# Optimization experiments

Measured on AMD Instinct MI355X. Metric: run time of the kernel, lower is better.

Reference implementation:

```python
import jax, jax.numpy as jnp
import numpy as np
from jax.scipy.special import logsumexp

D_MODEL = 512
NHEAD = 8
BATCH = 2
SEQ = 1024


def _safe_log_relu(v):
    # log(max(v, 0)) with well-defined (zero) gradient where v <= 0
    pos = v > 0
    return jnp.where(pos, jnp.log(jnp.where(pos, v, 1.0)), -jnp.inf)


def _split_heads(t, h):
    b, l, hd = t.shape
    return t.reshape(b, l, h, hd // h).transpose(0, 2, 1, 3)  # (B,H,L,d)


def setup_inputs() -> dict:
    key = jax.random.key(0)
    ks = jax.random.split(key, 9)
    s = 1.0 / np.sqrt(D_MODEL)
    x = jax.random.normal(ks[0], (BATCH, SEQ, D_MODEL), jnp.float32)
    mk = lambda k: jax.random.normal(k, (D_MODEL, D_MODEL), jnp.float32) * s
    mb = lambda k: jax.random.normal(k, (D_MODEL,), jnp.float32) * 0.02
    return {
        "x": x,
        "W_Q": mk(ks[1]), "b_Q": mb(ks[2]),
        "W_K": mk(ks[3]), "b_K": mb(ks[4]),
        "W_V": mk(ks[5]), "b_V": mb(ks[6]),
        "W_O": mk(ks[7]), "b_O": mb(ks[8]),
    }


def reference(x, W_Q, b_Q, W_K, b_K, W_V, b_V, W_O, b_O):
    # self-attention: queries = keys = values = x
    Q = _split_heads(x @ W_Q.T + b_Q, NHEAD)  # (B,H,L,D)
    K = _split_heads(x @ W_K.T + b_K, NHEAD)  # (B,H,L,D)
    V = _split_heads(x @ W_V.T + b_V, NHEAD)  # (B,H,L,Dv)

    # normalizer: log sum_j sum_d exp(Q_id) * exp(K_jd)
    log_B = logsumexp(Q + logsumexp(K, axis=-2, keepdims=True), axis=-1)  # (B,H,L)

    log_V_plus = _safe_log_relu(V)[..., None, :]    # (B,H,L,1,Dv)
    log_V_minus = _safe_log_relu(-V)[..., None, :]  # (B,H,L,1,Dv)

    # reduce over key positions: (B,H,L,D,Dv) -> (B,H,D,Dv)
    lse_KV_plus = logsumexp(K[..., :, :, None] + log_V_plus, axis=-3)
    lse_KV_minus = logsumexp(K[..., :, :, None] + log_V_minus, axis=-3)

    # reduce over feature dim D: (B,H,L,D,Dv) -> (B,H,L,Dv)
    log_A_plus = logsumexp(Q[..., None] + lse_KV_plus[..., None, :, :], axis=-2)
    log_A_minus = logsumexp(Q[..., None] + lse_KV_minus[..., None, :, :], axis=-2)

    heads = jnp.exp(log_A_plus - log_B[..., None]) - jnp.exp(log_A_minus - log_B[..., None])

    b, h, l, dv = heads.shape
    joined = heads.transpose(0, 2, 1, 3).reshape(b, l, h * dv)
    return joined @ W_O.T + b_O
```

## Files before the change

### kernel.cpp

```cpp
#include <hip/hip_runtime.h>
#include <math.h>

#define DM   512
#define NH   8
#define HD   64
#define B_   2
#define L_   1024
#define M_   (B_ * L_)

typedef __attribute__((ext_vector_type(8))) short  bfrag;
typedef __attribute__((ext_vector_type(4))) float  fv4;
typedef __attribute__((ext_vector_type(4))) unsigned short usv4;
typedef __attribute__((ext_vector_type(8))) unsigned short usv8;

__device__ __forceinline__ unsigned short f32_bf16_rne(float f) {
    unsigned u = __float_as_uint(f);
    unsigned r = u + 0x7FFF + ((u >> 16) & 1);
    return (unsigned short)(r >> 16);
}
__device__ __forceinline__ float bf16_f32(unsigned short h) {
    return __uint_as_float(((unsigned)h) << 16);
}

__device__ __forceinline__ void stage16(const unsigned short* g, unsigned short* l) {
    __builtin_amdgcn_global_load_lds(
        (const __attribute__((address_space(1))) void*)g,
        (__attribute__((address_space(3))) void*)l,
        16, 0, 0);
}

__global__ __launch_bounds__(256) void prep_kernel(
    const float* __restrict__ x,
    const float* __restrict__ Wq, const float* __restrict__ Wk,
    const float* __restrict__ Wv,
    unsigned short* __restrict__ xh, unsigned short* __restrict__ xl,
    unsigned short* __restrict__ wh, unsigned short* __restrict__ wl,
    float* __restrict__ zred) {
    int bid = blockIdx.x;
    if (bid >= 1792) {
        float4 zv = {0.f, 0.f, 0.f, 0.f};
        *(float4*)(zred + (size_t)threadIdx.x * 4) = zv;
        return;
    }
    const float* src; unsigned short *dh, *dl; size_t off;
    if (bid < 1024) {
        src = x; dh = xh; dl = xl; off = (size_t)bid * 1024;
    } else {
        int wsel = (bid - 1024) >> 8;
        int wb   = (bid - 1024) & 255;
        src = (wsel == 0) ? Wq : (wsel == 1) ? Wk : Wv;
        dh = wh + (size_t)wsel * 262144;
        dl = wl + (size_t)wsel * 262144;
        off = (size_t)wb * 1024;
    }
    size_t i = off + (size_t)threadIdx.x * 4;
    float4 v = *(const float4*)(src + i);
    usv4 h, l;
    h.x = f32_bf16_rne(v.x); l.x = f32_bf16_rne(v.x - bf16_f32(h.x));
    h.y = f32_bf16_rne(v.y); l.y = f32_bf16_rne(v.y - bf16_f32(h.y));
    h.z = f32_bf16_rne(v.z); l.z = f32_bf16_rne(v.z - bf16_f32(h.z));
    h.w = f32_bf16_rne(v.w); l.w = f32_bf16_rne(v.w - bf16_f32(h.w));
    *(usv4*)(dh + i) = h;
    *(usv4*)(dl + i) = l;
}

#define TM 64
#define TN 64
#define TK 32
#define LDA 32
#define NSTEP (DM / TK)

__device__ __forceinline__ void mfma_gemm_bf16(
    const unsigned short* __restrict__ Ahg, const unsigned short* __restrict__ Alg,
    const unsigned short* __restrict__ Bhg, const unsigned short* __restrict__ Blg,
    const float* __restrict__ bias, float* __restrict__ C, int do_exp,
    int m0, int n0) {
    __shared__ __align__(16) unsigned short Ah[2][TM * LDA];
    __shared__ __align__(16) unsigned short Al[2][TM * LDA];
    __shared__ __align__(16) unsigned short Bh[2][TN * LDA];
    __shared__ __align__(16) unsigned short Bl[2][TN * LDA];

    const int tid  = threadIdx.x;
    const int wave = tid >> 6, lane = tid & 63;
    const int quad = lane >> 4, r16 = lane & 15;

    const int srow = lane >> 2;
    const int scol = (lane & 3) << 3;
    const size_t gaBase = (size_t)(m0 + wave * 16 + srow) * DM + scol;
    const size_t gbBase = (size_t)(n0 + wave * 16 + srow) * DM + scol;
    const int ldst = wave * 512;

    fv4 acc[4] = {};

    stage16(Ahg + gaBase, &Ah[0][ldst]);
    stage16(Alg + gaBase, &Al[0][ldst]);
    stage16(Bhg + gbBase, &Bh[0][ldst]);
    stage16(Blg + gbBase, &Bl[0][ldst]);
    __syncthreads();

    int cur = 0;
    for (int t = 0; t < NSTEP; ++t) {
        if (t + 1 < NSTEP) {
            const size_t koff = (size_t)(t + 1) * TK;
            stage16(Ahg + gaBase + koff, &Ah[cur ^ 1][ldst]);
            stage16(Alg + gaBase + koff, &Al[cur ^ 1][ldst]);
            stage16(Bhg + gbBase + koff, &Bh[cur ^ 1][ldst]);
            stage16(Blg + gbBase + koff, &Bl[cur ^ 1][ldst]);
        }
        const int aoff = (wave * 16 + r16) * LDA + quad * 8;
        bfrag ah = *(const bfrag*)(&Ah[cur][aoff]);
        bfrag al = *(const bfrag*)(&Al[cur][aoff]);
        bfrag bh[4], bl[4];
#pragma unroll
        for (int j = 0; j < 4; ++j) {
            const int boff = (j * 16 + r16) * LDA + quad * 8;
            bh[j] = *(const bfrag*)(&Bh[cur][boff]);
            bl[j] = *(const bfrag*)(&Bl[cur][boff]);
        }
#pragma unroll
        for (int j = 0; j < 4; ++j) {
            acc[j] = __builtin_amdgcn_mfma_f32_16x16x32_bf16(ah, bh[j], acc[j], 0, 0, 0);
            acc[j] = __builtin_amdgcn_mfma_f32_16x16x32_bf16(ah, bl[j], acc[j], 0, 0, 0);
            acc[j] = __builtin_amdgcn_mfma_f32_16x16x32_bf16(al, bh[j], acc[j], 0, 0, 0);
        }
        __syncthreads();
        cur ^= 1;
    }

#pragma unroll
    for (int j = 0; j < 4; ++j) {
        int n = n0 + j * 16 + r16;
        float bn = bias[n];
#pragma unroll
        for (int r = 0; r < 4; ++r) {
            int m = m0 + wave * 16 + quad * 4 + r;
            float v = acc[j][r] + bn;
            if (do_exp) v = __expf(v);
            C[(size_t)m * DM + n] = v;
        }
    }
}

__global__ __launch_bounds__(256) void gemm_qkv_kernel(
    const unsigned short* __restrict__ xh, const unsigned short* __restrict__ xl,
    const unsigned short* __restrict__ wh, const unsigned short* __restrict__ wl,
    const float* __restrict__ bq, const float* __restrict__ bk, const float* __restrict__ bv,
    float* __restrict__ Qe, float* __restrict__ Ke, float* __restrict__ V) {
    int z = blockIdx.z;
    const float* b = (z == 0) ? bq : (z == 1) ? bk : bv;
    float* C = (z == 0) ? Qe : (z == 1) ? Ke : V;
    mfma_gemm_bf16(xh, xl, wh + (size_t)z * 262144, wl + (size_t)z * 262144,
                   b, C, z < 2, blockIdx.y * TM, blockIdx.x * TN);
}

__global__ __launch_bounds__(256) void gemm_out_kernel(
    const unsigned short* __restrict__ jh, const unsigned short* __restrict__ jl,
    const unsigned short* __restrict__ w2h, const unsigned short* __restrict__ w2l,
    const float* __restrict__ bo, float* __restrict__ C) {
    int b = blockIdx.y >> 4;
    mfma_gemm_bf16(jh, jl, w2h + (size_t)b * 262144, w2l + (size_t)b * 262144,
                   bo, C, 0, blockIdx.y * TM, blockIdx.x * TN);
}

#define JT 64
__global__ __launch_bounds__(256) void kv_stats_kernel(
    const float* __restrict__ Kbuf, const float* __restrict__ Vbuf,
    float* __restrict__ Spart, float* __restrict__ zred) {
    const int split = blockIdx.x, bh = blockIdx.y;
    const int b = bh >> 3, h = bh & 7;
    const int j0 = split * JT;

    __shared__ __align__(16) float EK[JT][HD + 4];
    __shared__ __align__(16) float VS[JT][HD + 4];

    const int tid = threadIdx.x;
#pragma unroll
    for (int t = 0; t < 4; ++t) {
        int idx = tid + t * 256;
        int r = idx >> 4;
        int c = (idx & 15) << 2;
        size_t row = (size_t)(b * L_ + j0 + r) * DM + h * HD + c;
        *(float4*)&EK[r][c] = *(const float4*)(Kbuf + row);
        *(float4*)&VS[r][c] = *(const float4*)(Vbuf + row);
    }
    __syncthreads();

    const int tx = tid & 15, ty = tid >> 4;
    float acc[4][4] = {{0.f}};
#pragma unroll 8
    for (int jj = 0; jj < JT; ++jj) {
        float4 ek = *(const float4*)&EK[jj][ty * 4];
        float4 vs = *(const float4*)&VS[jj][tx * 4];
        float e[4] = {ek.x, ek.y, ek.z, ek.w};
        float v[4] = {vs.x, vs.y, vs.z, vs.w};
#pragma unroll
        for (int i = 0; i < 4; ++i)
#pragma unroll
            for (int j = 0; j < 4; ++j) acc[i][j] += e[i] * v[j];
    }

    float* sp = Spart + ((size_t)bh * 16 + split) * (HD * HD);
#pragma unroll
    for (int i = 0; i < 4; ++i) {
        float4 o; o.x = acc[i][0]; o.y = acc[i][1]; o.z = acc[i][2]; o.w = acc[i][3];
        *(float4*)(sp + (ty * 4 + i) * HD + tx * 4) = o;
    }
    if (tid < HD) {
        float z = 0.f;
#pragma unroll 8
        for (int jj = 0; jj < JT; ++jj) z += EK[jj][tid];
        atomicAdd(zred + (size_t)bh * HD + tid, z);
    }
}

__global__ __launch_bounds__(256) void mid_kernel(
    const float* __restrict__ Spart, const float* __restrict__ zred,
    const float* __restrict__ Qbuf, const float* __restrict__ Wo,
    unsigned short* __restrict__ w2h, unsigned short* __restrict__ w2l,
    unsigned short* __restrict__ jh, unsigned short* __restrict__ jl) {
    const int tid = threadIdx.x;
    const int bid = blockIdx.x;
    if (bid < 128) {
        __shared__ __align__(16) float Sl[HD][HD + 4];
        __shared__ __align__(16) float Wol[HD][HD + 4];
        const int b = bid >> 6, r = bid & 63;
        const int h = r >> 3, nq = r & 7;
        const int n0 = nq * 64, bh = b * NH + h;
        const float* sp = Spart + (size_t)bh * 16 * (HD * HD);
#pragma unroll
        for (int t4 = 0; t4 < 4; ++t4) {
            int idx4 = tid + t4 * 256;
            const float* p0 = sp + (size_t)idx4 * 4;
            float4 s = {0.f, 0.f, 0.f, 0.f};
#pragma unroll
            for (int p = 0; p < 16; ++p) {
                float4 v = *(const float4*)(p0 + (size_t)p * (HD * HD));
                s.x += v.x; s.y += v.y; s.z += v.z; s.w += v.w;
            }
            int d = idx4 >> 4, e4 = (idx4 & 15) << 2;
            *(float4*)&Sl[d][e4] = s;
            *(float4*)&Wol[d][e4] =
                *(const float4*)(Wo + (size_t)(n0 + d) * DM + h * HD + e4);
        }
        __syncthreads();
        const int nl = tid & 15;
        const int d0 = tid >> 4;
        float acc[4][4] = {};
#pragma unroll
        for (int e4 = 0; e4 < 16; ++e4) {
            float4 w[4], s[4];
#pragma unroll
            for (int j = 0; j < 4; ++j) w[j] = *(const float4*)&Wol[nl + j * 16][e4 * 4];
#pragma unroll
            for (int i = 0; i < 4; ++i) s[i] = *(const float4*)&Sl[d0 + i * 16][e4 * 4];
#pragma unroll
            for (int j = 0; j < 4; ++j)
#pragma unroll
                for (int i = 0; i < 4; ++i)
                    acc[j][i] += w[j].x * s[i].x + w[j].y * s[i].y
                               + w[j].z * s[i].z + w[j].w * s[i].w;
        }
#pragma unroll
        for (int j = 0; j < 4; ++j) {
            int n = n0 + nl + j * 16;
#pragma unroll
            for (int i = 0; i < 4; ++i) {
                int d = d0 + i * 16;
                size_t addr = ((size_t)(b * DM + n)) * DM + h * HD + d;
                float v = acc[j][i];
                unsigned short hh = f32_bf16_rne(v);
                w2h[addr] = hh;
                w2l[addr] = f32_bf16_rne(v - bf16_f32(hh));
            }
        }
    } else {
        const int bid2 = bid - 128;
        const int w = tid >> 6, lane = tid & 63;
        const int b = bid2 >> 5;
        const int row0 = bid2 * 32 + w * 8;
        const float4 z0 = *(const float4*)(zred + (size_t)b * DM + lane * 8);
        const float4 z1 = *(const float4*)(zred + (size_t)b * DM + lane * 8 + 4);
#pragma unroll
        for (int rr = 0; rr < 8; ++rr) {
            const size_t rowoff = (size_t)(row0 + rr) * DM + lane * 8;
            float4 q0 = *(const float4*)(Qbuf + rowoff);
            float4 q1 = *(const float4*)(Qbuf + rowoff + 4);
            float part = q0.x * z0.x + q0.y * z0.y + q0.z * z0.z + q0.w * z0.w
                       + q1.x * z1.x + q1.y * z1.y + q1.z * z1.z + q1.w * z1.w;
            part += __shfl_xor(part, 1, 64);
            part += __shfl_xor(part, 2, 64);
            part += __shfl_xor(part, 4, 64);
            float inv = 1.0f / part;
            float v[8] = {q0.x * inv, q0.y * inv, q0.z * inv, q0.w * inv,
                          q1.x * inv, q1.y * inv, q1.z * inv, q1.w * inv};
            usv8 hv, lv;
#pragma unroll
            for (int k = 0; k < 8; ++k) {
                unsigned short hh = f32_bf16_rne(v[k]);
                hv[k] = hh;
                lv[k] = f32_bf16_rne(v[k] - bf16_f32(hh));
            }
            *(usv8*)(jh + rowoff) = hv;
            *(usv8*)(jl + rowoff) = lv;
        }
    }
}

extern "C" void kernel_launch(void* const* d_in, const int* in_sizes, int n_in,
                              void* d_out, int out_size, void* d_ws, size_t ws_size,
                              hipStream_t stream) {
    const float* x  = (const float*)d_in[0];
    const float* Wq = (const float*)d_in[1];
    const float* bq = (const float*)d_in[2];
    const float* Wk = (const float*)d_in[3];
    const float* bk = (const float*)d_in[4];
    const float* Wv = (const float*)d_in[5];
    const float* bv = (const float*)d_in[6];
    const float* Wo = (const float*)d_in[7];
    const float* bo = (const float*)d_in[8];
    float* out = (float*)d_out;

    float* f = (float*)d_ws;
    const size_t NQ = (size_t)M_ * DM;
    float* Qe    = f;
    float* Ke    = f + NQ;
    float* V     = f + 2 * NQ;
    float* Spart = f + 3 * NQ;
    float* zred  = f + 4 * NQ;
    unsigned short* u = (unsigned short*)(f + 4 * NQ + 1024);
    unsigned short* xh  = u;
    unsigned short* xl  = u + NQ;
    unsigned short* wh  = u + 2 * NQ;
    unsigned short* wl  = u + 2 * NQ + 786432;
    unsigned short* jh  = u + 2 * NQ + 2 * 786432;
    unsigned short* jl  = jh + NQ;
    unsigned short* w2h = jl + NQ;
    unsigned short* w2l = w2h + 524288;

    prep_kernel<<<1793, 256, 0, stream>>>(x, Wq, Wk, Wv, xh, xl, wh, wl, zred);

    dim3 gQKV(DM / TN, M_ / TM, 3);
    gemm_qkv_kernel<<<gQKV, 256, 0, stream>>>(xh, xl, wh, wl, bq, bk, bv, Qe, Ke, V);

    kv_stats_kernel<<<dim3(16, 16), 256, 0, stream>>>(Ke, V, Spart, zred);

    mid_kernel<<<192, 256, 0, stream>>>(Spart, zred, Qe, Wo, w2h, w2l, jh, jl);

    dim3 gO(DM / TN, M_ / TM, 1);
    gemm_out_kernel<<<gO, 256, 0, stream>>>(jh, jl, w2h, w2l, bo, out);
}
```

Measured before the change: 131.3 us.

## Fuse all five stages into one persistent kernel with software grid barriers

```diff
diff --git a/kernel.cpp b/kernel.cpp
--- a/kernel.cpp
+++ b/kernel.cpp
@@ -29,39 +29,24 @@
         16, 0, 0);
 }
 
-__global__ __launch_bounds__(256) void prep_kernel(
-    const float* __restrict__ x,
-    const float* __restrict__ Wq, const float* __restrict__ Wk,
-    const float* __restrict__ Wv,
-    unsigned short* __restrict__ xh, unsigned short* __restrict__ xl,
-    unsigned short* __restrict__ wh, unsigned short* __restrict__ wl,
-    float* __restrict__ zred) {
-    int bid = blockIdx.x;
-    if (bid >= 1792) {
-        float4 zv = {0.f, 0.f, 0.f, 0.f};
-        *(float4*)(zred + (size_t)threadIdx.x * 4) = zv;
-        return;
-    }
-    const float* src; unsigned short *dh, *dl; size_t off;
-    if (bid < 1024) {
-        src = x; dh = xh; dl = xl; off = (size_t)bid * 1024;
-    } else {
-        int wsel = (bid - 1024) >> 8;
-        int wb   = (bid - 1024) & 255;
-        src = (wsel == 0) ? Wq : (wsel == 1) ? Wk : Wv;
-        dh = wh + (size_t)wsel * 262144;
-        dl = wl + (size_t)wsel * 262144;
-        off = (size_t)wb * 1024;
-    }
-    size_t i = off + (size_t)threadIdx.x * 4;
-    float4 v = *(const float4*)(src + i);
-    usv4 h, l;
-    h.x = f32_bf16_rne(v.x); l.x = f32_bf16_rne(v.x - bf16_f32(h.x));
-    h.y = f32_bf16_rne(v.y); l.y = f32_bf16_rne(v.y - bf16_f32(h.y));
-    h.z = f32_bf16_rne(v.z); l.z = f32_bf16_rne(v.z - bf16_f32(h.z));
-    h.w = f32_bf16_rne(v.w); l.w = f32_bf16_rne(v.w - bf16_f32(h.w));
-    *(usv4*)(dh + i) = h;
-    *(usv4*)(dl + i) = l;
+#define GRID_N 256
+
+__device__ __forceinline__ void grid_barrier(unsigned* bar) {
+    __syncthreads();
+    if (threadIdx.x == 0) {
+        __threadfence();
+        unsigned g = __hip_atomic_load(bar + 1, __ATOMIC_RELAXED, __HIP_MEMORY_SCOPE_AGENT);
+        unsigned a = __hip_atomic_fetch_add(bar, 1u, __ATOMIC_ACQ_REL, __HIP_MEMORY_SCOPE_AGENT);
+        if (a == GRID_N - 1) {
+            __hip_atomic_store(bar, 0u, __ATOMIC_RELAXED, __HIP_MEMORY_SCOPE_AGENT);
+            __hip_atomic_store(bar + 1, g + 1u, __ATOMIC_RELEASE, __HIP_MEMORY_SCOPE_AGENT);
+        } else {
+            while (__hip_atomic_load(bar + 1, __ATOMIC_ACQUIRE, __HIP_MEMORY_SCOPE_AGENT) == g)
+                __builtin_amdgcn_s_sleep(2);
+        }
+        __threadfence();
+    }
+    __syncthreads();
 }
 
 #define TM 64
@@ -71,14 +56,15 @@
 #define NSTEP (DM / TK)
 
 __device__ __forceinline__ void mfma_gemm_bf16(
+    unsigned short* S,
     const unsigned short* __restrict__ Ahg, const unsigned short* __restrict__ Alg,
     const unsigned short* __restrict__ Bhg, const unsigned short* __restrict__ Blg,
     const float* __restrict__ bias, float* __restrict__ C, int do_exp,
     int m0, int n0) {
-    __shared__ __align__(16) unsigned short Ah[2][TM * LDA];
-    __shared__ __align__(16) unsigned short Al[2][TM * LDA];
-    __shared__ __align__(16) unsigned short Bh[2][TN * LDA];
-    __shared__ __align__(16) unsigned short Bl[2][TN * LDA];
+    unsigned short* Ah = S;
+    unsigned short* Al = S + 4096;
+    unsigned short* Bh = S + 8192;
+    unsigned short* Bl = S + 12288;
 
     const int tid  = threadIdx.x;
     const int wave = tid >> 6, lane = tid & 63;
@@ -92,30 +78,32 @@
 
     fv4 acc[4] = {};
 
-    stage16(Ahg + gaBase, &Ah[0][ldst]);
-    stage16(Alg + gaBase, &Al[0][ldst]);
-    stage16(Bhg + gbBase, &Bh[0][ldst]);
-    stage16(Blg + gbBase, &Bl[0][ldst]);
+    stage16(Ahg + gaBase, Ah + ldst);
+    stage16(Alg + gaBase, Al + ldst);
+    stage16(Bhg + gbBase, Bh + ldst);
+    stage16(Blg + gbBase, Bl + ldst);
     __syncthreads();
 
     int cur = 0;
     for (int t = 0; t < NSTEP; ++t) {
         if (t + 1 < NSTEP) {
             const size_t koff = (size_t)(t + 1) * TK;
-            stage16(Ahg + gaBase + koff, &Ah[cur ^ 1][ldst]);
-            stage16(Alg + gaBase + koff, &Al[cur ^ 1][ldst]);
-            stage16(Bhg + gbBase + koff, &Bh[cur ^ 1][ldst]);
-            stage16(Blg + gbBase + koff, &Bl[cur ^ 1][ldst]);
-        }
-        const int aoff = (wave * 16 + r16) * LDA + quad * 8;
-        bfrag ah = *(const bfrag*)(&Ah[cur][aoff]);
-        bfrag al = *(const bfrag*)(&Al[cur][aoff]);
+            const int d = (cur ^ 1) * 2048 + ldst;
+            stage16(Ahg + gaBase + koff, Ah + d);
+            stage16(Alg + gaBase + koff, Al + d);
+            stage16(Bhg + gbBase + koff, Bh + d);
+            stage16(Blg + gbBase + koff, Bl + d);
+        }
+        const int base = cur * 2048;
+        const int aoff = base + (wave * 16 + r16) * LDA + quad * 8;
+        bfrag ah = *(const bfrag*)(Ah + aoff);
+        bfrag al = *(const bfrag*)(Al + aoff);
         bfrag bh[4], bl[4];
 #pragma unroll
         for (int j = 0; j < 4; ++j) {
-            const int boff = (j * 16 + r16) * LDA + quad * 8;
-            bh[j] = *(const bfrag*)(&Bh[cur][boff]);
-            bl[j] = *(const bfrag*)(&Bl[cur][boff]);
+            const int boff = base + (j * 16 + r16) * LDA + quad * 8;
+            bh[j] = *(const bfrag*)(Bh + boff);
+            bl[j] = *(const bfrag*)(Bl + boff);
         }
 #pragma unroll
         for (int j = 0; j < 4; ++j) {
@@ -141,89 +129,130 @@
     }
 }
 
-__global__ __launch_bounds__(256) void gemm_qkv_kernel(
-    const unsigned short* __restrict__ xh, const unsigned short* __restrict__ xl,
-    const unsigned short* __restrict__ wh, const unsigned short* __restrict__ wl,
-    const float* __restrict__ bq, const float* __restrict__ bk, const float* __restrict__ bv,
-    float* __restrict__ Qe, float* __restrict__ Ke, float* __restrict__ V) {
-    int z = blockIdx.z;
-    const float* b = (z == 0) ? bq : (z == 1) ? bk : bv;
-    float* C = (z == 0) ? Qe : (z == 1) ? Ke : V;
-    mfma_gemm_bf16(xh, xl, wh + (size_t)z * 262144, wl + (size_t)z * 262144,
-                   b, C, z < 2, blockIdx.y * TM, blockIdx.x * TN);
-}
-
-__global__ __launch_bounds__(256) void gemm_out_kernel(
-    const unsigned short* __restrict__ jh, const unsigned short* __restrict__ jl,
-    const unsigned short* __restrict__ w2h, const unsigned short* __restrict__ w2l,
-    const float* __restrict__ bo, float* __restrict__ C) {
-    int b = blockIdx.y >> 4;
-    mfma_gemm_bf16(jh, jl, w2h + (size_t)b * 262144, w2l + (size_t)b * 262144,
-                   bo, C, 0, blockIdx.y * TM, blockIdx.x * TN);
-}
-
 #define JT 64
-__global__ __launch_bounds__(256) void kv_stats_kernel(
-    const float* __restrict__ Kbuf, const float* __restrict__ Vbuf,
-    float* __restrict__ Spart, float* __restrict__ zred) {
-    const int split = blockIdx.x, bh = blockIdx.y;
-    const int b = bh >> 3, h = bh & 7;
-    const int j0 = split * JT;
-
-    __shared__ __align__(16) float EK[JT][HD + 4];
-    __shared__ __align__(16) float VS[JT][HD + 4];
-
+
+__global__ __launch_bounds__(256, 2) void fused_kernel(
+    const float* __restrict__ x,
+    const float* __restrict__ Wq, const float* __restrict__ bq,
+    const float* __restrict__ Wk, const float* __restrict__ bk,
+    const float* __restrict__ Wv, const float* __restrict__ bv,
+    const float* __restrict__ Wo, const float* __restrict__ bo,
+    float* __restrict__ out, float* __restrict__ ws) {
+    __shared__ __align__(16) unsigned char SMEM[34816];
+
+    const size_t NQ = (size_t)M_ * DM;
+    float* Qe    = ws;
+    float* Ke    = ws + NQ;
+    float* V     = ws + 2 * NQ;
+    float* Spart = ws + 3 * NQ;
+    float* zred  = ws + 4 * NQ;
+    unsigned short* u = (unsigned short*)(ws + 4 * NQ + 1024);
+    unsigned short* xh  = u;
+    unsigned short* xl  = u + NQ;
+    unsigned short* wh  = u + 2 * NQ;
+    unsigned short* wl  = u + 2 * NQ + 786432;
+    unsigned short* jh  = u + 2 * NQ + 2 * 786432;
+    unsigned short* jl  = jh + NQ;
+    unsigned short* w2h = jl + NQ;
+    unsigned short* w2l = w2h + 524288;
+    unsigned* bar = (unsigned*)(w2l + 524288);
+
+    const int id  = blockIdx.x;
     const int tid = threadIdx.x;
-#pragma unroll
-    for (int t = 0; t < 4; ++t) {
-        int idx = tid + t * 256;
-        int r = idx >> 4;
-        int c = (idx & 15) << 2;
-        size_t row = (size_t)(b * L_ + j0 + r) * DM + h * HD + c;
-        *(float4*)&EK[r][c] = *(const float4*)(Kbuf + row);
-        *(float4*)&VS[r][c] = *(const float4*)(Vbuf + row);
-    }
-    __syncthreads();
-
-    const int tx = tid & 15, ty = tid >> 4;
-    float acc[4][4] = {{0.f}};
+
+    for (int c = id; c < 1793; c += GRID_N) {
+        if (c >= 1792) {
+            float4 zv = {0.f, 0.f, 0.f, 0.f};
+            *(float4*)(zred + (size_t)tid * 4) = zv;
+            continue;
+        }
+        const float* src; unsigned short *dh, *dl; size_t off;
+        if (c < 1024) {
+            src = x; dh = xh; dl = xl; off = (size_t)c * 1024;
+        } else {
+            int wsel = (c - 1024) >> 8;
+            int wb   = (c - 1024) & 255;
+            src = (wsel == 0) ? Wq : (wsel == 1) ? Wk : Wv;
+            dh = wh + (size_t)wsel * 262144;
+            dl = wl + (size_t)wsel * 262144;
+            off = (size_t)wb * 1024;
+        }
+        size_t i = off + (size_t)tid * 4;
+        float4 v = *(const float4*)(src + i);
+        usv4 h, l;
+        h.x = f32_bf16_rne(v.x); l.x = f32_bf16_rne(v.x - bf16_f32(h.x));
+        h.y = f32_bf16_rne(v.y); l.y = f32_bf16_rne(v.y - bf16_f32(h.y));
+        h.z = f32_bf16_rne(v.z); l.z = f32_bf16_rne(v.z - bf16_f32(h.z));
+        h.w = f32_bf16_rne(v.w); l.w = f32_bf16_rne(v.w - bf16_f32(h.w));
+        *(usv4*)(dh + i) = h;
+        *(usv4*)(dl + i) = l;
+    }
+    grid_barrier(bar);
+
+    {
+        const int m0 = (id >> 3) * TM;
+        const int n0 = (id & 7) * TN;
+#pragma unroll 1
+        for (int z = 0; z < 3; ++z) {
+            const float* bb = (z == 0) ? bq : (z == 1) ? bk : bv;
+            float* C = (z == 0) ? Qe : (z == 1) ? Ke : V;
+            mfma_gemm_bf16((unsigned short*)SMEM, xh, xl,
+                           wh + (size_t)z * 262144, wl + (size_t)z * 262144,
+                           bb, C, z < 2, m0, n0);
+        }
+    }
+    grid_barrier(bar);
+
+    {
+        float* EK = (float*)SMEM;
+        float* VS = EK + JT * (HD + 4);
+        const int split = id & 15, bh = id >> 4;
+        const int b = bh >> 3, h = bh & 7;
+        const int j0 = split * JT;
+#pragma unroll
+        for (int t = 0; t < 4; ++t) {
+            int idx = tid + t * 256;
+            int r = idx >> 4;
+            int c = (idx & 15) << 2;
+            size_t row = (size_t)(b * L_ + j0 + r) * DM + h * HD + c;
+            *(float4*)&EK[r * (HD + 4) + c] = *(const float4*)(Ke + row);
+            *(float4*)&VS[r * (HD + 4) + c] = *(const float4*)(V + row);
+        }
+        __syncthreads();
+
+        const int tx = tid & 15, ty = tid >> 4;
+        float acc[4][4] = {{0.f}};
 #pragma unroll 8
-    for (int jj = 0; jj < JT; ++jj) {
-        float4 ek = *(const float4*)&EK[jj][ty * 4];
-        float4 vs = *(const float4*)&VS[jj][tx * 4];
-        float e[4] = {ek.x, ek.y, ek.z, ek.w};
-        float v[4] = {vs.x, vs.y, vs.z, vs.w};
-#pragma unroll
-        for (int i = 0; i < 4; ++i)
-#pragma unroll
-            for (int j = 0; j < 4; ++j) acc[i][j] += e[i] * v[j];
-    }
-
-    float* sp = Spart + ((size_t)bh * 16 + split) * (HD * HD);
-#pragma unroll
-    for (int i = 0; i < 4; ++i) {
-        float4 o; o.x = acc[i][0]; o.y = acc[i][1]; o.z = acc[i][2]; o.w = acc[i][3];
-        *(float4*)(sp + (ty * 4 + i) * HD + tx * 4) = o;
-    }
-    if (tid < HD) {
-        float z = 0.f;
+        for (int jj = 0; jj < JT; ++jj) {
+            float4 ek = *(const float4*)&EK[jj * (HD + 4) + ty * 4];
+            float4 vs = *(const float4*)&VS[jj * (HD + 4) + tx * 4];
+            float e[4] = {ek.x, ek.y, ek.z, ek.w};
+            float v[4] = {vs.x, vs.y, vs.z, vs.w};
+#pragma unroll
+            for (int i = 0; i < 4; ++i)
+#pragma unroll
+                for (int j = 0; j < 4; ++j) acc[i][j] += e[i] * v[j];
+        }
+
+        float* sp = Spart + ((size_t)bh * 16 + split) * (HD * HD);
+#pragma unroll
+        for (int i = 0; i < 4; ++i) {
+            float4 o; o.x = acc[i][0]; o.y = acc[i][1]; o.z = acc[i][2]; o.w = acc[i][3];
+            *(float4*)(sp + (ty * 4 + i) * HD + tx * 4) = o;
+        }
+        if (tid < HD) {
+            float z = 0.f;
 #pragma unroll 8
-        for (int jj = 0; jj < JT; ++jj) z += EK[jj][tid];
-        atomicAdd(zred + (size_t)bh * HD + tid, z);
-    }
-}
-
-__global__ __launch_bounds__(256) void mid_kernel(
-    const float* __restrict__ Spart, const float* __restrict__ zred,
-    const float* __restrict__ Qbuf, const float* __restrict__ Wo,
-    unsigned short* __restrict__ w2h, unsigned short* __restrict__ w2l,
-    unsigned short* __restrict__ jh, unsigned short* __restrict__ jl) {
-    const int tid = threadIdx.x;
-    const int bid = blockIdx.x;
-    if (bid < 128) {
-        __shared__ __align__(16) float Sl[HD][HD + 4];
-        __shared__ __align__(16) float Wol[HD][HD + 4];
-        const int b = bid >> 6, r = bid & 63;
+            for (int jj = 0; jj < JT; ++jj) z += EK[jj * (HD + 4) + tid];
+            atomicAdd(zred + (size_t)bh * HD + tid, z);
+        }
+    }
+    grid_barrier(bar);
+
+    if (id < 128) {
+        float* Sl  = (float*)SMEM;
+        float* Wol = Sl + HD * (HD + 4);
+        const int b = id >> 6, r = id & 63;
         const int h = r >> 3, nq = r & 7;
         const int n0 = nq * 64, bh = b * NH + h;
         const float* sp = Spart + (size_t)bh * 16 * (HD * HD);
@@ -238,8 +267,8 @@
                 s.x += v.x; s.y += v.y; s.z += v.z; s.w += v.w;
             }
             int d = idx4 >> 4, e4 = (idx4 & 15) << 2;
-            *(float4*)&Sl[d][e4] = s;
-            *(float4*)&Wol[d][e4] =
+            *(float4*)&Sl[d * (HD + 4) + e4] = s;
+            *(float4*)&Wol[d * (HD + 4) + e4] =
                 *(const float4*)(Wo + (size_t)(n0 + d) * DM + h * HD + e4);
         }
         __syncthreads();
@@ -250,9 +279,11 @@
         for (int e4 = 0; e4 < 16; ++e4) {
             float4 w[4], s[4];
 #pragma unroll
-            for (int j = 0; j < 4; ++j) w[j] = *(const float4*)&Wol[nl + j * 16][e4 * 4];
-#pragma unroll
-            for (int i = 0; i < 4; ++i) s[i] = *(const float4*)&Sl[d0 + i * 16][e4 * 4];
+            for (int j = 0; j < 4; ++j)
+                w[j] = *(const float4*)&Wol[(nl + j * 16) * (HD + 4) + e4 * 4];
+#pragma unroll
+            for (int i = 0; i < 4; ++i)
+                s[i] = *(const float4*)&Sl[(d0 + i * 16) * (HD + 4) + e4 * 4];
 #pragma unroll
             for (int j = 0; j < 4; ++j)
 #pragma unroll
@@ -273,8 +304,8 @@
                 w2l[addr] = f32_bf16_rne(v - bf16_f32(hh));
             }
         }
-    } else {
-        const int bid2 = bid - 128;
+    } else if (id < 192) {
+        const int bid2 = id - 128;
         const int w = tid >> 6, lane = tid & 63;
         const int b = bid2 >> 5;
         const int row0 = bid2 * 32 + w * 8;
@@ -283,8 +314,8 @@
 #pragma unroll
         for (int rr = 0; rr < 8; ++rr) {
             const size_t rowoff = (size_t)(row0 + rr) * DM + lane * 8;
-            float4 q0 = *(const float4*)(Qbuf + rowoff);
-            float4 q1 = *(const float4*)(Qbuf + rowoff + 4);
+            float4 q0 = *(const float4*)(Qe + rowoff);
+            float4 q1 = *(const float4*)(Qe + rowoff + 4);
             float part = q0.x * z0.x + q0.y * z0.y + q0.z * z0.z + q0.w * z0.w
                        + q1.x * z1.x + q1.y * z1.y + q1.z * z1.z + q1.w * z1.w;
             part += __shfl_xor(part, 1, 64);
@@ -303,6 +334,17 @@
             *(usv8*)(jh + rowoff) = hv;
             *(usv8*)(jl + rowoff) = lv;
         }
+    }
+    grid_barrier(bar);
+
+    {
+        const int by = id >> 3;
+        const int b  = by >> 4;
+        const int m0 = by * TM;
+        const int n0 = (id & 7) * TN;
+        mfma_gemm_bf16((unsigned short*)SMEM, jh, jl,
+                       w2h + (size_t)b * 262144, w2l + (size_t)b * 262144,
+                       bo, out, 0, m0, n0);
     }
 }
 
@@ -319,33 +361,13 @@
     const float* Wo = (const float*)d_in[7];
     const float* bo = (const float*)d_in[8];
     float* out = (float*)d_out;
-
-    float* f = (float*)d_ws;
+    float* ws  = (float*)d_ws;
+
     const size_t NQ = (size_t)M_ * DM;
-    float* Qe    = f;
-    float* Ke    = f + NQ;
-    float* V     = f + 2 * NQ;
-    float* Spart = f + 3 * NQ;
-    float* zred  = f + 4 * NQ;
-    unsigned short* u = (unsigned short*)(f + 4 * NQ + 1024);
-    unsigned short* xh  = u;
-    unsigned short* xl  = u + NQ;
-    unsigned short* wh  = u + 2 * NQ;
-    unsigned short* wl  = u + 2 * NQ + 786432;
-    unsigned short* jh  = u + 2 * NQ + 2 * 786432;
-    unsigned short* jl  = jh + NQ;
-    unsigned short* w2h = jl + NQ;
-    unsigned short* w2l = w2h + 524288;
-
-    prep_kernel<<<1793, 256, 0, stream>>>(x, Wq, Wk, Wv, xh, xl, wh, wl, zred);
-
-    dim3 gQKV(DM / TN, M_ / TM, 3);
-    gemm_qkv_kernel<<<gQKV, 256, 0, stream>>>(xh, xl, wh, wl, bq, bk, bv, Qe, Ke, V);
-
-    kv_stats_kernel<<<dim3(16, 16), 256, 0, stream>>>(Ke, V, Spart, zred);
-
-    mid_kernel<<<192, 256, 0, stream>>>(Spart, zred, Qe, Wo, w2h, w2l, jh, jl);
-
-    dim3 gO(DM / TN, M_ / TM, 1);
-    gemm_out_kernel<<<gO, 256, 0, stream>>>(jh, jl, w2h, w2l, bo, out);
-}
+    unsigned short* u = (unsigned short*)(ws + 4 * NQ + 1024);
+    unsigned* bar = (unsigned*)(u + 2 * NQ + 2 * 786432 + 2 * NQ + 2 * 524288);
+    hipMemsetAsync((void*)bar, 0, 8, stream);
+
+    fused_kernel<<<dim3(GRID_N), dim3(256), 0, stream>>>(
+        x, Wq, bq, Wk, bk, Wv, bv, Wo, bo, out, ws);
+}
```

After: 319.7 us. 144% more time.

## Fuse fp32-to-bf16 hi/lo split into QKV GEMM, drop prep kernel

Applied to the files above, without the earlier changes.

```diff
diff --git a/kernel.cpp b/kernel.cpp
--- a/kernel.cpp
+++ b/kernel.cpp
@@ -22,6 +22,17 @@
     return __uint_as_float(((unsigned)h) << 16);
 }
 
+__device__ __forceinline__ void cvt8(const float4 a, const float4 b,
+                                     usv8* hi, usv8* lo) {
+    float f[8] = {a.x, a.y, a.z, a.w, b.x, b.y, b.z, b.w};
+#pragma unroll
+    for (int k = 0; k < 8; ++k) {
+        unsigned short h = f32_bf16_rne(f[k]);
+        (*hi)[k] = h;
+        (*lo)[k] = f32_bf16_rne(f[k] - bf16_f32(h));
+    }
+}
+
 __device__ __forceinline__ void stage16(const unsigned short* g, unsigned short* l) {
     __builtin_amdgcn_global_load_lds(
         (const __attribute__((address_space(1))) void*)g,
@@ -29,61 +40,131 @@
         16, 0, 0);
 }
 
-__global__ __launch_bounds__(256) void prep_kernel(
-    const float* __restrict__ x,
-    const float* __restrict__ Wq, const float* __restrict__ Wk,
-    const float* __restrict__ Wv,
-    unsigned short* __restrict__ xh, unsigned short* __restrict__ xl,
-    unsigned short* __restrict__ wh, unsigned short* __restrict__ wl,
-    float* __restrict__ zred) {
-    int bid = blockIdx.x;
-    if (bid >= 1792) {
-        float4 zv = {0.f, 0.f, 0.f, 0.f};
-        *(float4*)(zred + (size_t)threadIdx.x * 4) = zv;
-        return;
-    }
-    const float* src; unsigned short *dh, *dl; size_t off;
-    if (bid < 1024) {
-        src = x; dh = xh; dl = xl; off = (size_t)bid * 1024;
-    } else {
-        int wsel = (bid - 1024) >> 8;
-        int wb   = (bid - 1024) & 255;
-        src = (wsel == 0) ? Wq : (wsel == 1) ? Wk : Wv;
-        dh = wh + (size_t)wsel * 262144;
-        dl = wl + (size_t)wsel * 262144;
-        off = (size_t)wb * 1024;
-    }
-    size_t i = off + (size_t)threadIdx.x * 4;
-    float4 v = *(const float4*)(src + i);
-    usv4 h, l;
-    h.x = f32_bf16_rne(v.x); l.x = f32_bf16_rne(v.x - bf16_f32(h.x));
-    h.y = f32_bf16_rne(v.y); l.y = f32_bf16_rne(v.y - bf16_f32(h.y));
-    h.z = f32_bf16_rne(v.z); l.z = f32_bf16_rne(v.z - bf16_f32(h.z));
-    h.w = f32_bf16_rne(v.w); l.w = f32_bf16_rne(v.w - bf16_f32(h.w));
-    *(usv4*)(dh + i) = h;
-    *(usv4*)(dl + i) = l;
-}
-
 #define TM 64
 #define TN 64
 #define TK 32
 #define LDA 32
 #define NSTEP (DM / TK)
 
-__device__ __forceinline__ void mfma_gemm_bf16(
-    const unsigned short* __restrict__ Ahg, const unsigned short* __restrict__ Alg,
-    const unsigned short* __restrict__ Bhg, const unsigned short* __restrict__ Blg,
-    const float* __restrict__ bias, float* __restrict__ C, int do_exp,
-    int m0, int n0) {
+__global__ __launch_bounds__(256) void gemm_qkv_kernel(
+    const float* __restrict__ x,
+    const float* __restrict__ Wq, const float* __restrict__ Wk,
+    const float* __restrict__ Wv,
+    const float* __restrict__ bq, const float* __restrict__ bk,
+    const float* __restrict__ bv,
+    float* __restrict__ Qe, float* __restrict__ Ke, float* __restrict__ V,
+    float* __restrict__ zred) {
     __shared__ __align__(16) unsigned short Ah[2][TM * LDA];
     __shared__ __align__(16) unsigned short Al[2][TM * LDA];
     __shared__ __align__(16) unsigned short Bh[2][TN * LDA];
     __shared__ __align__(16) unsigned short Bl[2][TN * LDA];
 
+    const int z = blockIdx.z;
+    const float* W    = (z == 0) ? Wq : (z == 1) ? Wk : Wv;
+    const float* bias = (z == 0) ? bq : (z == 1) ? bk : bv;
+    float* C          = (z == 0) ? Qe : (z == 1) ? Ke : V;
+    const int m0 = blockIdx.y * TM, n0 = blockIdx.x * TN;
+    const int do_exp = (z < 2);
+
+    const int tid = threadIdx.x;
+    if (blockIdx.x == 0 && blockIdx.y == 0 && z == 0) {
+        float4 zv = {0.f, 0.f, 0.f, 0.f};
+        *(float4*)(zred + (size_t)tid * 4) = zv;
+    }
+
+    const int wave = tid >> 6, lane = tid & 63;
+    const int quad = lane >> 4, r16 = lane & 15;
+    const int srow = lane >> 2;
+    const int scol = (lane & 3) << 3;
+    const size_t gaBase = (size_t)(m0 + wave * 16 + srow) * DM + scol;
+    const size_t gbBase = (size_t)(n0 + wave * 16 + srow) * DM + scol;
+    const int soff = (wave * 16 + srow) * LDA + scol;
+
+    fv4 acc[4] = {};
+
+    {
+        float4 a0 = *(const float4*)(x + gaBase);
+        float4 a1 = *(const float4*)(x + gaBase + 4);
+        float4 b0 = *(const float4*)(W + gbBase);
+        float4 b1 = *(const float4*)(W + gbBase + 4);
+        usv8 h, l;
+        cvt8(a0, a1, &h, &l);
+        *(usv8*)(&Ah[0][soff]) = h; *(usv8*)(&Al[0][soff]) = l;
+        cvt8(b0, b1, &h, &l);
+        *(usv8*)(&Bh[0][soff]) = h; *(usv8*)(&Bl[0][soff]) = l;
+    }
+    __syncthreads();
+
+    int cur = 0;
+    for (int t = 0; t < NSTEP; ++t) {
+        float4 na0, na1, nb0, nb1;
+        if (t + 1 < NSTEP) {
+            const size_t k = (size_t)(t + 1) * TK;
+            na0 = *(const float4*)(x + gaBase + k);
+            na1 = *(const float4*)(x + gaBase + k + 4);
+            nb0 = *(const float4*)(W + gbBase + k);
+            nb1 = *(const float4*)(W + gbBase + k + 4);
+        }
+        const int aoff = (wave * 16 + r16) * LDA + quad * 8;
+        bfrag ah = *(const bfrag*)(&Ah[cur][aoff]);
+        bfrag al = *(const bfrag*)(&Al[cur][aoff]);
+        bfrag bh[4], bl[4];
+#pragma unroll
+        for (int j = 0; j < 4; ++j) {
+            const int boff = (j * 16 + r16) * LDA + quad * 8;
+            bh[j] = *(const bfrag*)(&Bh[cur][boff]);
+            bl[j] = *(const bfrag*)(&Bl[cur][boff]);
+        }
+#pragma unroll
+        for (int j = 0; j < 4; ++j) {
+            acc[j] = __builtin_amdgcn_mfma_f32_16x16x32_bf16(ah, bh[j], acc[j], 0, 0, 0);
+            acc[j] = __builtin_amdgcn_mfma_f32_16x16x32_bf16(ah, bl[j], acc[j], 0, 0, 0);
+            acc[j] = __builtin_amdgcn_mfma_f32_16x16x32_bf16(al, bh[j], acc[j], 0, 0, 0);
+        }
+        if (t + 1 < NSTEP) {
+            usv8 h, l;
+            cvt8(na0, na1, &h, &l);
+            *(usv8*)(&Ah[cur ^ 1][soff]) = h; *(usv8*)(&Al[cur ^ 1][soff]) = l;
+            cvt8(nb0, nb1, &h, &l);
+            *(usv8*)(&Bh[cur ^ 1][soff]) = h; *(usv8*)(&Bl[cur ^ 1][soff]) = l;
+        }
+        __syncthreads();
+        cur ^= 1;
+    }
+
+#pragma unroll
+    for (int j = 0; j < 4; ++j) {
+        int n = n0 + j * 16 + r16;
+        float bn = bias[n];
+#pragma unroll
+        for (int r = 0; r < 4; ++r) {
+            int m = m0 + wave * 16 + quad * 4 + r;
+            float v = acc[j][r] + bn;
+            if (do_exp) v = __expf(v);
+            C[(size_t)m * DM + n] = v;
+        }
+    }
+}
+
+__global__ __launch_bounds__(256) void gemm_out_kernel(
+    const unsigned short* __restrict__ jh, const unsigned short* __restrict__ jl,
+    const unsigned short* __restrict__ w2h, const unsigned short* __restrict__ w2l,
+    const float* __restrict__ bo, float* __restrict__ C) {
+    __shared__ __align__(16) unsigned short Ah[2][TM * LDA];
+    __shared__ __align__(16) unsigned short Al[2][TM * LDA];
+    __shared__ __align__(16) unsigned short Bh[2][TN * LDA];
+    __shared__ __align__(16) unsigned short Bl[2][TN * LDA];
+
+    const int bb = blockIdx.y >> 4;
+    const unsigned short* Ahg = jh;
+    const unsigned short* Alg = jl;
+    const unsigned short* Bhg = w2h + (size_t)bb * 262144;
+    const unsigned short* Blg = w2l + (size_t)bb * 262144;
+    const int m0 = blockIdx.y * TM, n0 = blockIdx.x * TN;
+
     const int tid  = threadIdx.x;
     const int wave = tid >> 6, lane = tid & 63;
     const int quad = lane >> 4, r16 = lane & 15;
-
     const int srow = lane >> 2;
     const int scol = (lane & 3) << 3;
     const size_t gaBase = (size_t)(m0 + wave * 16 + srow) * DM + scol;
@@ -130,36 +211,13 @@
 #pragma unroll
     for (int j = 0; j < 4; ++j) {
         int n = n0 + j * 16 + r16;
-        float bn = bias[n];
+        float bn = bo[n];
 #pragma unroll
         for (int r = 0; r < 4; ++r) {
             int m = m0 + wave * 16 + quad * 4 + r;
-            float v = acc[j][r] + bn;
-            if (do_exp) v = __expf(v);
-            C[(size_t)m * DM + n] = v;
-        }
-    }
-}
-
-__global__ __launch_bounds__(256) void gemm_qkv_kernel(
-    const unsigned short* __restrict__ xh, const unsigned short* __restrict__ xl,
-    const unsigned short* __restrict__ wh, const unsigned short* __restrict__ wl,
-    const float* __restrict__ bq, const float* __restrict__ bk, const float* __restrict__ bv,
-    float* __restrict__ Qe, float* __restrict__ Ke, float* __restrict__ V) {
-    int z = blockIdx.z;
-    const float* b = (z == 0) ? bq : (z == 1) ? bk : bv;
-    float* C = (z == 0) ? Qe : (z == 1) ? Ke : V;
-    mfma_gemm_bf16(xh, xl, wh + (size_t)z * 262144, wl + (size_t)z * 262144,
-                   b, C, z < 2, blockIdx.y * TM, blockIdx.x * TN);
-}
-
-__global__ __launch_bounds__(256) void gemm_out_kernel(
-    const unsigned short* __restrict__ jh, const unsigned short* __restrict__ jl,
-    const unsigned short* __restrict__ w2h, const unsigned short* __restrict__ w2l,
-    const float* __restrict__ bo, float* __restrict__ C) {
-    int b = blockIdx.y >> 4;
-    mfma_gemm_bf16(jh, jl, w2h + (size_t)b * 262144, w2l + (size_t)b * 262144,
-                   bo, C, 0, blockIdx.y * TM, blockIdx.x * TN);
+            C[(size_t)m * DM + n] = acc[j][r] + bn;
+        }
+    }
 }
 
 #define JT 64
@@ -328,19 +386,14 @@
     float* Spart = f + 3 * NQ;
     float* zred  = f + 4 * NQ;
     unsigned short* u = (unsigned short*)(f + 4 * NQ + 1024);
-    unsigned short* xh  = u;
-    unsigned short* xl  = u + NQ;
-    unsigned short* wh  = u + 2 * NQ;
-    unsigned short* wl  = u + 2 * NQ + 786432;
-    unsigned short* jh  = u + 2 * NQ + 2 * 786432;
+    unsigned short* jh  = u;
     unsigned short* jl  = jh + NQ;
     unsigned short* w2h = jl + NQ;
     unsigned short* w2l = w2h + 524288;
 
-    prep_kernel<<<1793, 256, 0, stream>>>(x, Wq, Wk, Wv, xh, xl, wh, wl, zred);
-
     dim3 gQKV(DM / TN, M_ / TM, 3);
-    gemm_qkv_kernel<<<gQKV, 256, 0, stream>>>(xh, xl, wh, wl, bq, bk, bv, Qe, Ke, V);
+    gemm_qkv_kernel<<<gQKV, 256, 0, stream>>>(x, Wq, Wk, Wv, bq, bk, bv,
+                                              Qe, Ke, V, zred);
 
     kv_stats_kernel<<<dim3(16, 16), 256, 0, stream>>>(Ke, V, Spart, zred);
 
```

Result: no change. 131.3 us, median of 2 (-0.0%).
